# Kernel optimization log

Measured on AMD Instinct MI355X. Metric: run time of the kernel, lower is better.

The kernel has to match this reference:

```python
import jax, jax.numpy as jnp
import numpy as np

E = 8        # num experts
K = 2        # top-k
H = 1024     # hidden size
F = 3584     # intermediate (ffn) size
B, S = 1, 2048


def setup_inputs() -> dict:
    key = jax.random.key(0)
    ks = jax.random.split(key, 5)
    scale_h = 1.0 / np.sqrt(H)
    scale_f = 1.0 / np.sqrt(F)
    return {
        "hidden_states": jax.random.normal(ks[0], (B, S, H), jnp.float32),
        "gate_w": jax.random.normal(ks[1], (E, H), jnp.float32) * scale_h,  # Linear [out,in]
        "w1": jax.random.normal(ks[2], (E, F, H), jnp.float32) * scale_h,
        "w3": jax.random.normal(ks[3], (E, F, H), jnp.float32) * scale_h,
        "w2": jax.random.normal(ks[4], (E, H, F), jnp.float32) * scale_f,
    }


def reference(hidden_states, gate_w, w1, w3, w2):
    b, s, h = hidden_states.shape
    x = hidden_states.reshape(-1, h)                       # [T,H]
    T = x.shape[0]
    # Router: softmax over experts, top-k, renormalize
    router_logits = x @ gate_w.T                           # [T,E]
    routing_weights = jax.nn.softmax(router_logits.astype(jnp.float32), axis=-1)
    topk_w, topk_idx = jax.lax.top_k(routing_weights, K)   # [T,K]
    topk_w = topk_w / jnp.sum(topk_w, axis=-1, keepdims=True)
    # Per-token, per-expert combine weight (0 for unselected experts) --
    # matches the original mask-and-sum over all experts.
    tok = jnp.arange(T)
    expert_weights = jnp.zeros((T, E), jnp.float32).at[tok[:, None], topk_idx].add(topk_w)  # [T,E]
    # Dense per-expert SiLU-gated MLP over all tokens (as the reference loop does),
    # vectorized across experts.
    g = jnp.einsum("th,efh->etf", x, w1)                   # [E,T,F]
    u = jnp.einsum("th,efh->etf", x, w3)                   # [E,T,F]
    act = jax.nn.silu(g) * u                               # [E,T,F]
    y = jnp.einsum("etf,ehf->eth", act, w2)                # [E,T,H]
    out = jnp.einsum("eth,te->th", y, expert_weights.astype(y.dtype))  # [T,H]
    return out.reshape(b, s, h)
```

## Files before the change

### kernel.cpp

```cpp
#include <hip/hip_runtime.h>
#include <hip/hip_bf16.h>

#define T_TOK 2048
#define HID   1024
#define FF    3584
#define NE    8
#define TOPK  2
#define GRIDY 40

typedef __bf16 bf16x8 __attribute__((ext_vector_type(8)));
typedef float  f32x4  __attribute__((ext_vector_type(4)));
typedef unsigned short u16x8 __attribute__((ext_vector_type(8)));

#define WS_COUNTS   0u
#define WS_OFFSETS  64u
#define WS_TILECNT  128u
#define WS_TLE      256u
#define WS_TLM      512u
#define WS_TOPKI    1024u
#define WS_TOPKW    17408u
#define WS_SLOTPOS  33792u
#define WS_SLOTROW  50176u
#define WS_ROUTETOK 66560u
#define WS_XBF      131072u
#define WS_ACT      (WS_XBF + 2048u*1024u*2u)
#define WS_Y        (WS_ACT + 4096u*3584u*2u)

static __device__ __forceinline__ unsigned short f2bf(float f) {
    unsigned int u = __builtin_bit_cast(unsigned int, f);
    u += 0x7FFFu + ((u >> 16) & 1u);
    return (unsigned short)(u >> 16);
}
static __device__ __forceinline__ unsigned int pack2(float a, float b) {
    unsigned int ua = __builtin_bit_cast(unsigned int, a) + 0x8000u;
    unsigned int ub = __builtin_bit_cast(unsigned int, b) + 0x8000u;
    return (ua >> 16) | (ub & 0xFFFF0000u);
}

__global__ void k_cvt_x(const float* __restrict__ x, unsigned short* __restrict__ xb) {
    int i = blockIdx.x * blockDim.x + threadIdx.x;
    float4 v = ((const float4*)x)[i];
    ushort4 o;
    o.x = f2bf(v.x); o.y = f2bf(v.y); o.z = f2bf(v.z); o.w = f2bf(v.w);
    ((ushort4*)xb)[i] = o;
}

__global__ void k_router(const float* __restrict__ x, const float* __restrict__ gw,
                         int* __restrict__ counts, int* __restrict__ topki,
                         float* __restrict__ topkw, int* __restrict__ slotpos) {
    int t = blockIdx.x;
    int l = threadIdx.x;
    const float* xr = x + (size_t)t * HID;
    float acc[NE];
#pragma unroll
    for (int e = 0; e < NE; ++e) acc[e] = 0.f;
#pragma unroll
    for (int i = 0; i < HID / 64; ++i) {
        int h = l + 64 * i;
        float xv = xr[h];
#pragma unroll
        for (int e = 0; e < NE; ++e) acc[e] += xv * gw[e * HID + h];
    }
#pragma unroll
    for (int e = 0; e < NE; ++e) {
#pragma unroll
        for (int off = 32; off; off >>= 1) acc[e] += __shfl_xor(acc[e], off);
    }
    if (l == 0) {
        float best = -1e30f, second = -1e30f;
        int bi = 0, si = 0;
#pragma unroll
        for (int e = 0; e < NE; ++e) {
            float v = acc[e];
            if (v > best) { second = best; si = bi; best = v; bi = e; }
            else if (v > second) { second = v; si = e; }
        }
        float w0 = 1.f / (1.f + __expf(second - best));
        float w1 = 1.f - w0;
        topki[2 * t] = bi;  topki[2 * t + 1] = si;
        topkw[2 * t] = w0;  topkw[2 * t + 1] = w1;
        slotpos[2 * t]     = atomicAdd(&counts[bi], 1);
        slotpos[2 * t + 1] = atomicAdd(&counts[si], 1);
    }
}

__global__ void k_prefix(const int* __restrict__ counts, int* __restrict__ offsets,
                         int* __restrict__ tle, int* __restrict__ tlm,
                         int* __restrict__ tilecnt) {
    if (threadIdx.x == 0) {
        int o = 0;
#pragma unroll
        for (int e = 0; e < NE; ++e) { offsets[e] = o; o += counts[e]; }
        int n = 0;
        for (int e = 0; e < NE; ++e) {
            int t = (counts[e] + 127) >> 7;
            for (int i = 0; i < t; ++i) { tle[n] = e; tlm[n] = i; ++n; }
        }
        tilecnt[0] = n;
    }
}

__global__ void k_fill(const int* __restrict__ topki, const int* __restrict__ slotpos,
                       const int* __restrict__ offsets, int* __restrict__ routetok,
                       int* __restrict__ slotrow) {
    int j = blockIdx.x * blockDim.x + threadIdx.x;
    if (j >= T_TOK * TOPK) return;
    int e = topki[j];
    int row = offsets[e] + slotpos[j];
    routetok[row] = j >> 1;
    slotrow[j] = row;
}

__global__ __launch_bounds__(256) void k_gemm1(
    const unsigned short* __restrict__ xb, const float* __restrict__ w1,
    const float* __restrict__ w3, const int* __restrict__ counts,
    const int* __restrict__ offsets, const int* __restrict__ routetok,
    const int* __restrict__ tle, const int* __restrict__ tlm,
    const int* __restrict__ tilecnt, unsigned short* __restrict__ act)
{
    int by = blockIdx.y;
    if (by >= tilecnt[0]) return;
    int e = tle[by], mtile = tlm[by];
    int cnt = counts[e], obase = offsets[e];
    int rbase = mtile * 128;
    int fbase = blockIdx.x * 64;

    __shared__ __align__(16) unsigned short lA[128 * 72];
    __shared__ __align__(16) unsigned short lB1[64 * 72];
    __shared__ __align__(16) unsigned short lB3[64 * 72];
    __shared__ int ltok[128];

    int tid = threadIdx.x;
    if (tid < 128) {
        int r = rbase + tid;
        ltok[tid] = (r < cnt) ? routetok[obase + r] : 0;
    }
    __syncthreads();

    const int ra0 = tid >> 3, ca = (tid & 7) * 8;
    const int rb0 = tid >> 4, cb = (tid & 15) * 4;
    const unsigned short* pa[4];
    const float* pb1[4];
    const float* pb3[4];
    const float* w1e = w1 + ((size_t)e * FF + fbase) * HID;
    const float* w3e = w3 + ((size_t)e * FF + fbase) * HID;
#pragma unroll
    for (int i = 0; i < 4; ++i) {
        pa[i]  = xb + (size_t)ltok[ra0 + 32 * i] * HID + ca;
        pb1[i] = w1e + (size_t)(rb0 + 16 * i) * HID + cb;
        pb3[i] = w3e + (size_t)(rb0 + 16 * i) * HID + cb;
    }

    int lane = tid & 63, wv = tid >> 6, wr = wv >> 1, wc = wv & 1;
    f32x4 accg[4][2], accu[4][2];
#pragma unroll
    for (int m = 0; m < 4; ++m)
#pragma unroll
        for (int n = 0; n < 2; ++n) {
            accg[m][n] = (f32x4){0.f, 0.f, 0.f, 0.f};
            accu[m][n] = (f32x4){0.f, 0.f, 0.f, 0.f};
        }

    u16x8 ra[4]; float4 r1[4], r3[4];
#pragma unroll
    for (int i = 0; i < 4; ++i) {
        ra[i] = *(const u16x8*)(pa[i]);
        r1[i] = *(const float4*)(pb1[i]);
        r3[i] = *(const float4*)(pb3[i]);
    }

    for (int kt = 0; kt < HID / 64; ++kt) {
#pragma unroll
        for (int i = 0; i < 4; ++i) {
            *(u16x8*)(lA + (ra0 + 32 * i) * 72 + ca) = ra[i];
            uint2 p1; p1.x = pack2(r1[i].x, r1[i].y); p1.y = pack2(r1[i].z, r1[i].w);
            uint2 p3; p3.x = pack2(r3[i].x, r3[i].y); p3.y = pack2(r3[i].z, r3[i].w);
            *(uint2*)(lB1 + (rb0 + 16 * i) * 72 + cb) = p1;
            *(uint2*)(lB3 + (rb0 + 16 * i) * 72 + cb) = p3;
        }
        __syncthreads();
        if (kt < HID / 64 - 1) {
            int kof = (kt + 1) * 64;
#pragma unroll
            for (int i = 0; i < 4; ++i) {
                ra[i] = *(const u16x8*)(pa[i] + kof);
                r1[i] = *(const float4*)(pb1[i] + kof);
                r3[i] = *(const float4*)(pb3[i] + kof);
            }
        }
#pragma unroll
        for (int kk = 0; kk < 64; kk += 32) {
            int kcol = kk + (lane >> 4) * 8;
            bf16x8 a[4], b1[2], b3[2];
#pragma unroll
            for (int m = 0; m < 4; ++m)
                a[m] = *(const bf16x8*)(lA + (wr * 64 + m * 16 + (lane & 15)) * 72 + kcol);
#pragma unroll
            for (int n = 0; n < 2; ++n) {
                b1[n] = *(const bf16x8*)(lB1 + (wc * 32 + n * 16 + (lane & 15)) * 72 + kcol);
                b3[n] = *(const bf16x8*)(lB3 + (wc * 32 + n * 16 + (lane & 15)) * 72 + kcol);
            }
#pragma unroll
            for (int m = 0; m < 4; ++m)
#pragma unroll
                for (int n = 0; n < 2; ++n) {
                    accg[m][n] = __builtin_amdgcn_mfma_f32_16x16x32_bf16(a[m], b1[n], accg[m][n], 0, 0, 0);
                    accu[m][n] = __builtin_amdgcn_mfma_f32_16x16x32_bf16(a[m], b3[n], accu[m][n], 0, 0, 0);
                }
        }
        __syncthreads();
    }

#pragma unroll
    for (int m = 0; m < 4; ++m)
#pragma unroll
        for (int n = 0; n < 2; ++n)
#pragma unroll
            for (int r = 0; r < 4; ++r) {
                int lr = wr * 64 + m * 16 + (lane >> 4) * 4 + r;
                if (rbase + lr < cnt) {
                    float g = accg[m][n][r], u = accu[m][n][r];
                    float s = g / (1.f + __expf(-g));
                    int col = fbase + wc * 32 + n * 16 + (lane & 15);
                    act[(size_t)(obase + rbase + lr) * FF + col] = f2bf(s * u);
                }
            }
}

__global__ __launch_bounds__(256) void k_gemm2(
    const unsigned short* __restrict__ act, const float* __restrict__ w2,
    const int* __restrict__ counts, const int* __restrict__ offsets,
    const int* __restrict__ tle, const int* __restrict__ tlm,
    const int* __restrict__ tilecnt, float* __restrict__ y)
{
    int by = blockIdx.y;
    if (by >= tilecnt[0]) return;
    int e = tle[by], mtile = tlm[by];
    int cnt = counts[e], obase = offsets[e];
    int rbase = mtile * 128;
    int hbase = blockIdx.x * 64;
    int z = blockIdx.z;
    const int KS = FF / 64 / 2;

    __shared__ __align__(16) unsigned short lA[128 * 72];
    __shared__ __align__(16) unsigned short lB[64 * 72];

    int tid = threadIdx.x;
    const int ra0 = tid >> 3, ca = (tid & 7) * 8;
    const int rb0 = tid >> 4, cb = (tid & 15) * 4;
    const unsigned short* pa[4];
    const float* pb[4];
    const float* w2e = w2 + ((size_t)e * HID + hbase) * FF;
    int kbase0 = z * KS * 64;
#pragma unroll
    for (int i = 0; i < 4; ++i) {
        int rowg = obase + rbase + ra0 + 32 * i;
        if (rowg > 4095) rowg = 4095;
        pa[i] = act + (size_t)rowg * FF + ca + kbase0;
        pb[i] = w2e + (size_t)(rb0 + 16 * i) * FF + cb + kbase0;
    }

    int lane = tid & 63, wv = tid >> 6, wr = wv >> 1, wc = wv & 1;
    f32x4 acc[4][2];
#pragma unroll
    for (int m = 0; m < 4; ++m)
#pragma unroll
        for (int n = 0; n < 2; ++n) acc[m][n] = (f32x4){0.f, 0.f, 0.f, 0.f};

    u16x8 ra[4]; float4 rb[4];
#pragma unroll
    for (int i = 0; i < 4; ++i) {
        ra[i] = *(const u16x8*)(pa[i]);
        rb[i] = *(const float4*)(pb[i]);
    }

    for (int kt = 0; kt < KS; ++kt) {
#pragma unroll
        for (int i = 0; i < 4; ++i) {
            *(u16x8*)(lA + (ra0 + 32 * i) * 72 + ca) = ra[i];
            uint2 p; p.x = pack2(rb[i].x, rb[i].y); p.y = pack2(rb[i].z, rb[i].w);
            *(uint2*)(lB + (rb0 + 16 * i) * 72 + cb) = p;
        }
        __syncthreads();
        if (kt < KS - 1) {
            int kof = (kt + 1) * 64;
#pragma unroll
            for (int i = 0; i < 4; ++i) {
                ra[i] = *(const u16x8*)(pa[i] + kof);
                rb[i] = *(const float4*)(pb[i] + kof);
            }
        }
#pragma unroll
        for (int kk = 0; kk < 64; kk += 32) {
            int kcol = kk + (lane >> 4) * 8;
            bf16x8 a[4], b[2];
#pragma unroll
            for (int m = 0; m < 4; ++m)
                a[m] = *(const bf16x8*)(lA + (wr * 64 + m * 16 + (lane & 15)) * 72 + kcol);
#pragma unroll
            for (int n = 0; n < 2; ++n)
                b[n] = *(const bf16x8*)(lB + (wc * 32 + n * 16 + (lane & 15)) * 72 + kcol);
#pragma unroll
            for (int m = 0; m < 4; ++m)
#pragma unroll
                for (int n = 0; n < 2; ++n)
                    acc[m][n] = __builtin_amdgcn_mfma_f32_16x16x32_bf16(a[m], b[n], acc[m][n], 0, 0, 0);
        }
        __syncthreads();
    }

    float* yz = y + (size_t)z * T_TOK * TOPK * HID;
#pragma unroll
    for (int m = 0; m < 4; ++m)
#pragma unroll
        for (int n = 0; n < 2; ++n)
#pragma unroll
            for (int r = 0; r < 4; ++r) {
                int lr = wr * 64 + m * 16 + (lane >> 4) * 4 + r;
                if (rbase + lr < cnt) {
                    int col = hbase + wc * 32 + n * 16 + (lane & 15);
                    yz[(size_t)(obase + rbase + lr) * HID + col] = acc[m][n][r];
                }
            }
}

__global__ void k_combine(const float* __restrict__ y, const int* __restrict__ slotrow,
                          const float* __restrict__ topkw, float* __restrict__ out) {
    int j = blockIdx.x * blockDim.x + threadIdx.x;
    int t = j >> 8, c = j & 255;
    int r0 = slotrow[2 * t], r1 = slotrow[2 * t + 1];
    float w0 = topkw[2 * t], w1 = topkw[2 * t + 1];
    const float4* y0 = (const float4*)y;
    const float4* y1 = (const float4*)(y + (size_t)T_TOK * TOPK * HID);
    float4 a0 = y0[(size_t)r0 * 256 + c], a1 = y1[(size_t)r0 * 256 + c];
    float4 b0 = y0[(size_t)r1 * 256 + c], b1 = y1[(size_t)r1 * 256 + c];
    float4 o;
    o.x = w0 * (a0.x + a1.x) + w1 * (b0.x + b1.x);
    o.y = w0 * (a0.y + a1.y) + w1 * (b0.y + b1.y);
    o.z = w0 * (a0.z + a1.z) + w1 * (b0.z + b1.z);
    o.w = w0 * (a0.w + a1.w) + w1 * (b0.w + b1.w);
    ((float4*)out)[j] = o;
}

extern "C" void kernel_launch(void* const* d_in, const int* in_sizes, int n_in,
                              void* d_out, int out_size, void* d_ws, size_t ws_size,
                              hipStream_t stream) {
    const float* x  = (const float*)d_in[0];
    const float* gw = (const float*)d_in[1];
    const float* w1 = (const float*)d_in[2];
    const float* w3 = (const float*)d_in[3];
    const float* w2 = (const float*)d_in[4];
    float* out = (float*)d_out;

    char* ws = (char*)d_ws;
    int*   counts   = (int*)(ws + WS_COUNTS);
    int*   offsets  = (int*)(ws + WS_OFFSETS);
    int*   tilecnt  = (int*)(ws + WS_TILECNT);
    int*   tle      = (int*)(ws + WS_TLE);
    int*   tlm      = (int*)(ws + WS_TLM);
    int*   topki    = (int*)(ws + WS_TOPKI);
    float* topkw    = (float*)(ws + WS_TOPKW);
    int*   slotpos  = (int*)(ws + WS_SLOTPOS);
    int*   slotrow  = (int*)(ws + WS_SLOTROW);
    int*   routetok = (int*)(ws + WS_ROUTETOK);
    unsigned short* xb   = (unsigned short*)(ws + WS_XBF);
    unsigned short* actb = (unsigned short*)(ws + WS_ACT);
    float* yb = (float*)(ws + WS_Y);

    hipMemsetAsync(counts, 0, 64, stream);
    k_cvt_x<<<2048, 256, 0, stream>>>(x, xb);
    k_router<<<T_TOK, 64, 0, stream>>>(x, gw, counts, topki, topkw, slotpos);
    k_prefix<<<1, 64, 0, stream>>>(counts, offsets, tle, tlm, tilecnt);
    k_fill<<<16, 256, 0, stream>>>(topki, slotpos, offsets, routetok, slotrow);
    k_gemm1<<<dim3(FF / 64, GRIDY, 1), 256, 0, stream>>>(xb, w1, w3, counts, offsets, routetok, tle, tlm, tilecnt, actb);
    k_gemm2<<<dim3(HID / 64, GRIDY, 2), 256, 0, stream>>>(actb, w2, counts, offsets, tle, tlm, tilecnt, yb);
    k_combine<<<2048, 256, 0, stream>>>(yb, slotrow, topkw, out);
}
```

Measured before the change: 285.5 us.

## Enlarge MoE GEMM tiles, load activations directly to registers, fuse x cast into router

Both expert GEMMs are retiled with larger per-expert M tiles (512 rows for gate/up, 256 for down) and 512-thread blocks. The A operand (tokens or activations) is now loaded straight from global memory into MFMA registers instead of staged through LDS. Only the fp32 weights still go through LDS, so each weight tile is reused across more tokens. The x-to-bf16 conversion is folded into the router kernel, which now processes four tokens per block, removing one launch. The trade-offs are heavier register use (16 accumulator tiles each for gate and up), uncoalesced gathered A loads, and fewer blocks, which may hurt occupancy when tiles are partly empty.

```diff
diff --git a/kernel.cpp b/kernel.cpp
--- a/kernel.cpp
+++ b/kernel.cpp
@@ -6,7 +6,6 @@
 #define FF    3584
 #define NE    8
 #define TOPK  2
-#define GRIDY 40
 
 typedef __bf16 bf16x8 __attribute__((ext_vector_type(8)));
 typedef float  f32x4  __attribute__((ext_vector_type(4)));
@@ -15,13 +14,15 @@
 #define WS_COUNTS   0u
 #define WS_OFFSETS  64u
 #define WS_TILECNT  128u
-#define WS_TLE      256u
-#define WS_TLM      512u
-#define WS_TOPKI    1024u
-#define WS_TOPKW    17408u
-#define WS_SLOTPOS  33792u
-#define WS_SLOTROW  50176u
-#define WS_ROUTETOK 66560u
+#define WS_TLE1     256u
+#define WS_TLM1     512u
+#define WS_TLE2     768u
+#define WS_TLM2     1024u
+#define WS_TOPKI    4096u
+#define WS_TOPKW    20480u
+#define WS_SLOTPOS  36864u
+#define WS_SLOTROW  53248u
+#define WS_ROUTETOK 69632u
 #define WS_XBF      131072u
 #define WS_ACT      (WS_XBF + 2048u*1024u*2u)
 #define WS_Y        (WS_ACT + 4096u*3584u*2u)
@@ -37,29 +38,30 @@
     return (ua >> 16) | (ub & 0xFFFF0000u);
 }
 
-__global__ void k_cvt_x(const float* __restrict__ x, unsigned short* __restrict__ xb) {
-    int i = blockIdx.x * blockDim.x + threadIdx.x;
-    float4 v = ((const float4*)x)[i];
-    ushort4 o;
-    o.x = f2bf(v.x); o.y = f2bf(v.y); o.z = f2bf(v.z); o.w = f2bf(v.w);
-    ((ushort4*)xb)[i] = o;
-}
-
-__global__ void k_router(const float* __restrict__ x, const float* __restrict__ gw,
-                         int* __restrict__ counts, int* __restrict__ topki,
-                         float* __restrict__ topkw, int* __restrict__ slotpos) {
-    int t = blockIdx.x;
-    int l = threadIdx.x;
+__global__ __launch_bounds__(256) void k_router(
+    const float* __restrict__ x, const float* __restrict__ gw,
+    unsigned short* __restrict__ xb, int* __restrict__ counts,
+    int* __restrict__ topki, float* __restrict__ topkw, int* __restrict__ slotpos)
+{
+    int t = blockIdx.x * 4 + (threadIdx.x >> 6);
+    int l = threadIdx.x & 63;
     const float* xr = x + (size_t)t * HID;
+    unsigned short* xbr = xb + (size_t)t * HID;
     float acc[NE];
 #pragma unroll
     for (int e = 0; e < NE; ++e) acc[e] = 0.f;
 #pragma unroll
-    for (int i = 0; i < HID / 64; ++i) {
-        int h = l + 64 * i;
-        float xv = xr[h];
-#pragma unroll
-        for (int e = 0; e < NE; ++e) acc[e] += xv * gw[e * HID + h];
+    for (int i = 0; i < 4; ++i) {
+        int h = l * 4 + i * 256;
+        float4 xv = *(const float4*)(xr + h);
+        ushort4 o;
+        o.x = f2bf(xv.x); o.y = f2bf(xv.y); o.z = f2bf(xv.z); o.w = f2bf(xv.w);
+        *(ushort4*)(xbr + h) = o;
+#pragma unroll
+        for (int e = 0; e < NE; ++e) {
+            float4 g = *(const float4*)(gw + e * HID + h);
+            acc[e] += xv.x * g.x + xv.y * g.y + xv.z * g.z + xv.w * g.w;
+        }
     }
 #pragma unroll
     for (int e = 0; e < NE; ++e) {
@@ -85,18 +87,21 @@
 }
 
 __global__ void k_prefix(const int* __restrict__ counts, int* __restrict__ offsets,
-                         int* __restrict__ tle, int* __restrict__ tlm,
+                         int* __restrict__ tl1e, int* __restrict__ tl1m,
+                         int* __restrict__ tl2e, int* __restrict__ tl2m,
                          int* __restrict__ tilecnt) {
     if (threadIdx.x == 0) {
         int o = 0;
 #pragma unroll
         for (int e = 0; e < NE; ++e) { offsets[e] = o; o += counts[e]; }
-        int n = 0;
+        int n1 = 0, n2 = 0;
         for (int e = 0; e < NE; ++e) {
-            int t = (counts[e] + 127) >> 7;
-            for (int i = 0; i < t; ++i) { tle[n] = e; tlm[n] = i; ++n; }
-        }
-        tilecnt[0] = n;
+            int t1 = (counts[e] + 511) >> 9;
+            for (int i = 0; i < t1; ++i) { tl1e[n1] = e; tl1m[n1] = i; ++n1; }
+            int t2 = (counts[e] + 255) >> 8;
+            for (int i = 0; i < t2; ++i) { tl2e[n2] = e; tl2m[n2] = i; ++n2; }
+        }
+        tilecnt[0] = n1; tilecnt[1] = n2;
     }
 }
 
@@ -111,101 +116,117 @@
     slotrow[j] = row;
 }
 
-__global__ __launch_bounds__(256) void k_gemm1(
+__global__ __launch_bounds__(512, 2) void k_gemm1(
     const unsigned short* __restrict__ xb, const float* __restrict__ w1,
     const float* __restrict__ w3, const int* __restrict__ counts,
     const int* __restrict__ offsets, const int* __restrict__ routetok,
-    const int* __restrict__ tle, const int* __restrict__ tlm,
+    const int* __restrict__ tl1e, const int* __restrict__ tl1m,
     const int* __restrict__ tilecnt, unsigned short* __restrict__ act)
 {
     int by = blockIdx.y;
     if (by >= tilecnt[0]) return;
-    int e = tle[by], mtile = tlm[by];
+    int e = tl1e[by];
+    int rbase = tl1m[by] * 512;
     int cnt = counts[e], obase = offsets[e];
-    int rbase = mtile * 128;
     int fbase = blockIdx.x * 64;
 
-    __shared__ __align__(16) unsigned short lA[128 * 72];
     __shared__ __align__(16) unsigned short lB1[64 * 72];
     __shared__ __align__(16) unsigned short lB3[64 * 72];
-    __shared__ int ltok[128];
+    __shared__ int ltok[512];
 
     int tid = threadIdx.x;
-    if (tid < 128) {
+    {
         int r = rbase + tid;
-        ltok[tid] = (r < cnt) ? routetok[obase + r] : 0;
+        int rc = r < cnt ? r : cnt - 1;
+        ltok[tid] = routetok[obase + rc];
     }
     __syncthreads();
 
-    const int ra0 = tid >> 3, ca = (tid & 7) * 8;
-    const int rb0 = tid >> 4, cb = (tid & 15) * 4;
-    const unsigned short* pa[4];
-    const float* pb1[4];
-    const float* pb3[4];
-    const float* w1e = w1 + ((size_t)e * FF + fbase) * HID;
-    const float* w3e = w3 + ((size_t)e * FF + fbase) * HID;
-#pragma unroll
-    for (int i = 0; i < 4; ++i) {
-        pa[i]  = xb + (size_t)ltok[ra0 + 32 * i] * HID + ca;
-        pb1[i] = w1e + (size_t)(rb0 + 16 * i) * HID + cb;
-        pb3[i] = w3e + (size_t)(rb0 + 16 * i) * HID + cb;
-    }
-
-    int lane = tid & 63, wv = tid >> 6, wr = wv >> 1, wc = wv & 1;
-    f32x4 accg[4][2], accu[4][2];
+    int lane = tid & 63, wv = tid >> 6;
+    int klane = (lane >> 4) * 8;
+    const char* xbb = (const char*)xb;
+    unsigned int aoff[4];
 #pragma unroll
     for (int m = 0; m < 4; ++m)
-#pragma unroll
-        for (int n = 0; n < 2; ++n) {
+        aoff[m] = (unsigned int)ltok[wv * 64 + m * 16 + (lane & 15)] * (HID * 2);
+
+    int rbr = tid >> 3, cbc = (tid & 7) * 8;
+    const float* pb1 = w1 + ((size_t)e * FF + fbase + rbr) * HID + cbc;
+    const float* pb3 = w3 + ((size_t)e * FF + fbase + rbr) * HID + cbc;
+
+    f32x4 accg[4][4], accu[4][4];
+#pragma unroll
+    for (int m = 0; m < 4; ++m)
+#pragma unroll
+        for (int n = 0; n < 4; ++n) {
             accg[m][n] = (f32x4){0.f, 0.f, 0.f, 0.f};
             accu[m][n] = (f32x4){0.f, 0.f, 0.f, 0.f};
         }
 
-    u16x8 ra[4]; float4 r1[4], r3[4];
-#pragma unroll
-    for (int i = 0; i < 4; ++i) {
-        ra[i] = *(const u16x8*)(pa[i]);
-        r1[i] = *(const float4*)(pb1[i]);
-        r3[i] = *(const float4*)(pb3[i]);
-    }
+    float4 r1a = *(const float4*)(pb1);
+    float4 r1b = *(const float4*)(pb1 + 4);
+    float4 r3a = *(const float4*)(pb3);
+    float4 r3b = *(const float4*)(pb3 + 4);
+    u16x8 a0[4], a1[4];
+#pragma unroll
+    for (int m = 0; m < 4; ++m)
+        a0[m] = *(const u16x8*)(xbb + aoff[m] + klane * 2);
 
     for (int kt = 0; kt < HID / 64; ++kt) {
-#pragma unroll
-        for (int i = 0; i < 4; ++i) {
-            *(u16x8*)(lA + (ra0 + 32 * i) * 72 + ca) = ra[i];
-            uint2 p1; p1.x = pack2(r1[i].x, r1[i].y); p1.y = pack2(r1[i].z, r1[i].w);
-            uint2 p3; p3.x = pack2(r3[i].x, r3[i].y); p3.y = pack2(r3[i].z, r3[i].w);
-            *(uint2*)(lB1 + (rb0 + 16 * i) * 72 + cb) = p1;
-            *(uint2*)(lB3 + (rb0 + 16 * i) * 72 + cb) = p3;
-        }
+        uint2 p;
+        p.x = pack2(r1a.x, r1a.y); p.y = pack2(r1a.z, r1a.w);
+        *(uint2*)(lB1 + rbr * 72 + cbc) = p;
+        p.x = pack2(r1b.x, r1b.y); p.y = pack2(r1b.z, r1b.w);
+        *(uint2*)(lB1 + rbr * 72 + cbc + 4) = p;
+        p.x = pack2(r3a.x, r3a.y); p.y = pack2(r3a.z, r3a.w);
+        *(uint2*)(lB3 + rbr * 72 + cbc) = p;
+        p.x = pack2(r3b.x, r3b.y); p.y = pack2(r3b.z, r3b.w);
+        *(uint2*)(lB3 + rbr * 72 + cbc + 4) = p;
         __syncthreads();
+
+        int kof = (kt + 1) * 64;
         if (kt < HID / 64 - 1) {
-            int kof = (kt + 1) * 64;
-#pragma unroll
-            for (int i = 0; i < 4; ++i) {
-                ra[i] = *(const u16x8*)(pa[i] + kof);
-                r1[i] = *(const float4*)(pb1[i] + kof);
-                r3[i] = *(const float4*)(pb3[i] + kof);
+            r1a = *(const float4*)(pb1 + kof);
+            r1b = *(const float4*)(pb1 + kof + 4);
+            r3a = *(const float4*)(pb3 + kof);
+            r3b = *(const float4*)(pb3 + kof + 4);
+        }
+#pragma unroll
+        for (int m = 0; m < 4; ++m)
+            a1[m] = *(const u16x8*)(xbb + aoff[m] + (kt * 64 + 32 + klane) * 2);
+        {
+            bf16x8 b1f[4], b3f[4];
+#pragma unroll
+            for (int n = 0; n < 4; ++n) {
+                b1f[n] = *(const bf16x8*)(lB1 + (n * 16 + (lane & 15)) * 72 + klane);
+                b3f[n] = *(const bf16x8*)(lB3 + (n * 16 + (lane & 15)) * 72 + klane);
             }
-        }
-#pragma unroll
-        for (int kk = 0; kk < 64; kk += 32) {
-            int kcol = kk + (lane >> 4) * 8;
-            bf16x8 a[4], b1[2], b3[2];
 #pragma unroll
             for (int m = 0; m < 4; ++m)
-                a[m] = *(const bf16x8*)(lA + (wr * 64 + m * 16 + (lane & 15)) * 72 + kcol);
-#pragma unroll
-            for (int n = 0; n < 2; ++n) {
-                b1[n] = *(const bf16x8*)(lB1 + (wc * 32 + n * 16 + (lane & 15)) * 72 + kcol);
-                b3[n] = *(const bf16x8*)(lB3 + (wc * 32 + n * 16 + (lane & 15)) * 72 + kcol);
+#pragma unroll
+                for (int n = 0; n < 4; ++n) {
+                    accg[m][n] = __builtin_amdgcn_mfma_f32_16x16x32_bf16(a0[m], b1f[n], accg[m][n], 0, 0, 0);
+                    accu[m][n] = __builtin_amdgcn_mfma_f32_16x16x32_bf16(a0[m], b3f[n], accu[m][n], 0, 0, 0);
+                }
+        }
+        if (kt < HID / 64 - 1) {
+#pragma unroll
+            for (int m = 0; m < 4; ++m)
+                a0[m] = *(const u16x8*)(xbb + aoff[m] + (kof + klane) * 2);
+        }
+        {
+            bf16x8 b1f[4], b3f[4];
+#pragma unroll
+            for (int n = 0; n < 4; ++n) {
+                b1f[n] = *(const bf16x8*)(lB1 + (n * 16 + (lane & 15)) * 72 + 32 + klane);
+                b3f[n] = *(const bf16x8*)(lB3 + (n * 16 + (lane & 15)) * 72 + 32 + klane);
             }
 #pragma unroll
             for (int m = 0; m < 4; ++m)
 #pragma unroll
-                for (int n = 0; n < 2; ++n) {
-                    accg[m][n] = __builtin_amdgcn_mfma_f32_16x16x32_bf16(a[m], b1[n], accg[m][n], 0, 0, 0);
-                    accu[m][n] = __builtin_amdgcn_mfma_f32_16x16x32_bf16(a[m], b3[n], accu[m][n], 0, 0, 0);
+                for (int n = 0; n < 4; ++n) {
+                    accg[m][n] = __builtin_amdgcn_mfma_f32_16x16x32_bf16(a1[m], b1f[n], accg[m][n], 0, 0, 0);
+                    accu[m][n] = __builtin_amdgcn_mfma_f32_16x16x32_bf16(a1[m], b3f[n], accu[m][n], 0, 0, 0);
                 }
         }
         __syncthreads();
@@ -214,111 +235,129 @@
 #pragma unroll
     for (int m = 0; m < 4; ++m)
 #pragma unroll
-        for (int n = 0; n < 2; ++n)
+        for (int n = 0; n < 4; ++n)
 #pragma unroll
             for (int r = 0; r < 4; ++r) {
-                int lr = wr * 64 + m * 16 + (lane >> 4) * 4 + r;
+                int lr = wv * 64 + m * 16 + (lane >> 4) * 4 + r;
                 if (rbase + lr < cnt) {
                     float g = accg[m][n][r], u = accu[m][n][r];
                     float s = g / (1.f + __expf(-g));
-                    int col = fbase + wc * 32 + n * 16 + (lane & 15);
+                    int col = fbase + n * 16 + (lane & 15);
                     act[(size_t)(obase + rbase + lr) * FF + col] = f2bf(s * u);
                 }
             }
 }
 
-__global__ __launch_bounds__(256) void k_gemm2(
+__global__ __launch_bounds__(512, 2) void k_gemm2(
     const unsigned short* __restrict__ act, const float* __restrict__ w2,
     const int* __restrict__ counts, const int* __restrict__ offsets,
-    const int* __restrict__ tle, const int* __restrict__ tlm,
+    const int* __restrict__ tl2e, const int* __restrict__ tl2m,
     const int* __restrict__ tilecnt, float* __restrict__ y)
 {
     int by = blockIdx.y;
-    if (by >= tilecnt[0]) return;
-    int e = tle[by], mtile = tlm[by];
+    if (by >= tilecnt[1]) return;
+    int e = tl2e[by];
+    int rbase = tl2m[by] * 256;
     int cnt = counts[e], obase = offsets[e];
-    int rbase = mtile * 128;
-    int hbase = blockIdx.x * 64;
+    int hbase = blockIdx.x * 128;
     int z = blockIdx.z;
-    const int KS = FF / 64 / 2;
-
-    __shared__ __align__(16) unsigned short lA[128 * 72];
-    __shared__ __align__(16) unsigned short lB[64 * 72];
-
-    int tid = threadIdx.x;
-    const int ra0 = tid >> 3, ca = (tid & 7) * 8;
-    const int rb0 = tid >> 4, cb = (tid & 15) * 4;
-    const unsigned short* pa[4];
-    const float* pb[4];
-    const float* w2e = w2 + ((size_t)e * HID + hbase) * FF;
-    int kbase0 = z * KS * 64;
-#pragma unroll
-    for (int i = 0; i < 4; ++i) {
-        int rowg = obase + rbase + ra0 + 32 * i;
-        if (rowg > 4095) rowg = 4095;
-        pa[i] = act + (size_t)rowg * FF + ca + kbase0;
-        pb[i] = w2e + (size_t)(rb0 + 16 * i) * FF + cb + kbase0;
-    }
-
-    int lane = tid & 63, wv = tid >> 6, wr = wv >> 1, wc = wv & 1;
-    f32x4 acc[4][2];
-#pragma unroll
-    for (int m = 0; m < 4; ++m)
-#pragma unroll
-        for (int n = 0; n < 2; ++n) acc[m][n] = (f32x4){0.f, 0.f, 0.f, 0.f};
-
-    u16x8 ra[4]; float4 rb[4];
-#pragma unroll
-    for (int i = 0; i < 4; ++i) {
-        ra[i] = *(const u16x8*)(pa[i]);
-        rb[i] = *(const float4*)(pb[i]);
-    }
+    const int kb0 = z * (FF / 2);
+    const int KS = FF / 2 / 64;
+
+    __shared__ __align__(16) unsigned short lB[128 * 72];
+
+    int tid = threadIdx.x, lane = tid & 63, wv = tid >> 6;
+    int klane = (lane >> 4) * 8;
+
+    int rbr = tid >> 2, cbc = (tid & 3) * 16;
+    const float* pb = w2 + ((size_t)e * HID + hbase + rbr) * FF + kb0 + cbc;
+
+    const char* actb = (const char*)act;
+    unsigned int aoff[2];
+#pragma unroll
+    for (int m = 0; m < 2; ++m) {
+        int r = obase + rbase + wv * 32 + m * 16 + (lane & 15);
+        if (r > 4095) r = 4095;
+        aoff[m] = (unsigned int)r * (FF * 2);
+    }
+
+    f32x4 acc[2][8];
+#pragma unroll
+    for (int m = 0; m < 2; ++m)
+#pragma unroll
+        for (int n = 0; n < 8; ++n) acc[m][n] = (f32x4){0.f, 0.f, 0.f, 0.f};
+
+    float4 rw0 = *(const float4*)(pb);
+    float4 rw1 = *(const float4*)(pb + 4);
+    float4 rw2 = *(const float4*)(pb + 8);
+    float4 rw3 = *(const float4*)(pb + 12);
+    u16x8 a0[2], a1[2];
+#pragma unroll
+    for (int m = 0; m < 2; ++m)
+        a0[m] = *(const u16x8*)(actb + aoff[m] + (kb0 + klane) * 2);
 
     for (int kt = 0; kt < KS; ++kt) {
-#pragma unroll
-        for (int i = 0; i < 4; ++i) {
-            *(u16x8*)(lA + (ra0 + 32 * i) * 72 + ca) = ra[i];
-            uint2 p; p.x = pack2(rb[i].x, rb[i].y); p.y = pack2(rb[i].z, rb[i].w);
-            *(uint2*)(lB + (rb0 + 16 * i) * 72 + cb) = p;
-        }
+        uint2 p;
+        p.x = pack2(rw0.x, rw0.y); p.y = pack2(rw0.z, rw0.w);
+        *(uint2*)(lB + rbr * 72 + cbc) = p;
+        p.x = pack2(rw1.x, rw1.y); p.y = pack2(rw1.z, rw1.w);
+        *(uint2*)(lB + rbr * 72 + cbc + 4) = p;
+        p.x = pack2(rw2.x, rw2.y); p.y = pack2(rw2.z, rw2.w);
+        *(uint2*)(lB + rbr * 72 + cbc + 8) = p;
+        p.x = pack2(rw3.x, rw3.y); p.y = pack2(rw3.z, rw3.w);
+        *(uint2*)(lB + rbr * 72 + cbc + 12) = p;
         __syncthreads();
+
+        int kof = (kt + 1) * 64;
         if (kt < KS - 1) {
-            int kof = (kt + 1) * 64;
-#pragma unroll
-            for (int i = 0; i < 4; ++i) {
-                ra[i] = *(const u16x8*)(pa[i] + kof);
-                rb[i] = *(const float4*)(pb[i] + kof);
-            }
-        }
-#pragma unroll
-        for (int kk = 0; kk < 64; kk += 32) {
-            int kcol = kk + (lane >> 4) * 8;
-            bf16x8 a[4], b[2];
-#pragma unroll
-            for (int m = 0; m < 4; ++m)
-                a[m] = *(const bf16x8*)(lA + (wr * 64 + m * 16 + (lane & 15)) * 72 + kcol);
-#pragma unroll
-            for (int n = 0; n < 2; ++n)
-                b[n] = *(const bf16x8*)(lB + (wc * 32 + n * 16 + (lane & 15)) * 72 + kcol);
-#pragma unroll
-            for (int m = 0; m < 4; ++m)
-#pragma unroll
-                for (int n = 0; n < 2; ++n)
-                    acc[m][n] = __builtin_amdgcn_mfma_f32_16x16x32_bf16(a[m], b[n], acc[m][n], 0, 0, 0);
+            rw0 = *(const float4*)(pb + kof);
+            rw1 = *(const float4*)(pb + kof + 4);
+            rw2 = *(const float4*)(pb + kof + 8);
+            rw3 = *(const float4*)(pb + kof + 12);
+        }
+#pragma unroll
+        for (int m = 0; m < 2; ++m)
+            a1[m] = *(const u16x8*)(actb + aoff[m] + (kb0 + kt * 64 + 32 + klane) * 2);
+        {
+            bf16x8 bf[8];
+#pragma unroll
+            for (int n = 0; n < 8; ++n)
+                bf[n] = *(const bf16x8*)(lB + (n * 16 + (lane & 15)) * 72 + klane);
+#pragma unroll
+            for (int m = 0; m < 2; ++m)
+#pragma unroll
+                for (int n = 0; n < 8; ++n)
+                    acc[m][n] = __builtin_amdgcn_mfma_f32_16x16x32_bf16(a0[m], bf[n], acc[m][n], 0, 0, 0);
+        }
+        if (kt < KS - 1) {
+#pragma unroll
+            for (int m = 0; m < 2; ++m)
+                a0[m] = *(const u16x8*)(actb + aoff[m] + (kb0 + kof + klane) * 2);
+        }
+        {
+            bf16x8 bf[8];
+#pragma unroll
+            for (int n = 0; n < 8; ++n)
+                bf[n] = *(const bf16x8*)(lB + (n * 16 + (lane & 15)) * 72 + 32 + klane);
+#pragma unroll
+            for (int m = 0; m < 2; ++m)
+#pragma unroll
+                for (int n = 0; n < 8; ++n)
+                    acc[m][n] = __builtin_amdgcn_mfma_f32_16x16x32_bf16(a1[m], bf[n], acc[m][n], 0, 0, 0);
         }
         __syncthreads();
     }
 
-    float* yz = y + (size_t)z * T_TOK * TOPK * HID;
-#pragma unroll
-    for (int m = 0; m < 4; ++m)
-#pragma unroll
-        for (int n = 0; n < 2; ++n)
+    float* yz = y + (size_t)z * (T_TOK * TOPK * HID);
+#pragma unroll
+    for (int m = 0; m < 2; ++m)
+#pragma unroll
+        for (int n = 0; n < 8; ++n)
 #pragma unroll
             for (int r = 0; r < 4; ++r) {
-                int lr = wr * 64 + m * 16 + (lane >> 4) * 4 + r;
+                int lr = wv * 32 + m * 16 + (lane >> 4) * 4 + r;
                 if (rbase + lr < cnt) {
-                    int col = hbase + wc * 32 + n * 16 + (lane & 15);
+                    int col = hbase + n * 16 + (lane & 15);
                     yz[(size_t)(obase + rbase + lr) * HID + col] = acc[m][n][r];
                 }
             }
@@ -356,8 +395,10 @@
     int*   counts   = (int*)(ws + WS_COUNTS);
     int*   offsets  = (int*)(ws + WS_OFFSETS);
     int*   tilecnt  = (int*)(ws + WS_TILECNT);
-    int*   tle      = (int*)(ws + WS_TLE);
-    int*   tlm      = (int*)(ws + WS_TLM);
+    int*   tl1e     = (int*)(ws + WS_TLE1);
+    int*   tl1m     = (int*)(ws + WS_TLM1);
+    int*   tl2e     = (int*)(ws + WS_TLE2);
+    int*   tl2m     = (int*)(ws + WS_TLM2);
     int*   topki    = (int*)(ws + WS_TOPKI);
     float* topkw    = (float*)(ws + WS_TOPKW);
     int*   slotpos  = (int*)(ws + WS_SLOTPOS);
@@ -368,11 +409,10 @@
     float* yb = (float*)(ws + WS_Y);
 
     hipMemsetAsync(counts, 0, 64, stream);
-    k_cvt_x<<<2048, 256, 0, stream>>>(x, xb);
-    k_router<<<T_TOK, 64, 0, stream>>>(x, gw, counts, topki, topkw, slotpos);
-    k_prefix<<<1, 64, 0, stream>>>(counts, offsets, tle, tlm, tilecnt);
+    k_router<<<T_TOK / 4, 256, 0, stream>>>(x, gw, xb, counts, topki, topkw, slotpos);
+    k_prefix<<<1, 64, 0, stream>>>(counts, offsets, tl1e, tl1m, tl2e, tl2m, tilecnt);
     k_fill<<<16, 256, 0, stream>>>(topki, slotpos, offsets, routetok, slotrow);
-    k_gemm1<<<dim3(FF / 64, GRIDY, 1), 256, 0, stream>>>(xb, w1, w3, counts, offsets, routetok, tle, tlm, tilecnt, actb);
-    k_gemm2<<<dim3(HID / 64, GRIDY, 2), 256, 0, stream>>>(actb, w2, counts, offsets, tle, tlm, tilecnt, yb);
+    k_gemm1<<<dim3(FF / 64, 16, 1), 512, 0, stream>>>(xb, w1, w3, counts, offsets, routetok, tl1e, tl1m, tilecnt, actb);
+    k_gemm2<<<dim3(HID / 128, 24, 2), 512, 0, stream>>>(actb, w2, counts, offsets, tl2e, tl2m, tilecnt, yb);
     k_combine<<<2048, 256, 0, stream>>>(yb, slotrow, topkw, out);
 }
```

Result: slower. 355.5 us (+24.5%).

## Double MoE GEMM row tiles to 256, pre-gather routed tokens, vectorize router

Applied to the files above, without the earlier changes.

Both expert GEMMs now use 256-row M tiles with 512-thread blocks instead of 128-row tiles with 256 threads. The tile list and grid height shrink to match, so each expert's fp32 weights are re-read from memory by fewer tiles. A new gather kernel writes routed tokens as contiguous bf16 rows, replacing the full x conversion and the per-tile indirect token lookup. The router now handles four tokens per block using float4 loads. In exchange the blocks need more LDS and registers, and padding in partially filled 256-row tiles wastes more compute.

```diff
diff --git a/kernel.cpp b/kernel.cpp
--- a/kernel.cpp
+++ b/kernel.cpp
@@ -6,7 +6,7 @@
 #define FF    3584
 #define NE    8
 #define TOPK  2
-#define GRIDY 40
+#define GRIDY 24
 
 typedef __bf16 bf16x8 __attribute__((ext_vector_type(8)));
 typedef float  f32x4  __attribute__((ext_vector_type(4)));
@@ -17,13 +17,13 @@
 #define WS_TILECNT  128u
 #define WS_TLE      256u
 #define WS_TLM      512u
-#define WS_TOPKI    1024u
-#define WS_TOPKW    17408u
-#define WS_SLOTPOS  33792u
-#define WS_SLOTROW  50176u
-#define WS_ROUTETOK 66560u
-#define WS_XBF      131072u
-#define WS_ACT      (WS_XBF + 2048u*1024u*2u)
+#define WS_TOPKI    4096u
+#define WS_TOPKW    20480u
+#define WS_SLOTPOS  36864u
+#define WS_SLOTROW  53248u
+#define WS_ROUTETOK 69632u
+#define WS_XG       131072u
+#define WS_ACT      (WS_XG + 4096u*1024u*2u)
 #define WS_Y        (WS_ACT + 4096u*3584u*2u)
 
 static __device__ __forceinline__ unsigned short f2bf(float f) {
@@ -37,29 +37,26 @@
     return (ua >> 16) | (ub & 0xFFFF0000u);
 }
 
-__global__ void k_cvt_x(const float* __restrict__ x, unsigned short* __restrict__ xb) {
-    int i = blockIdx.x * blockDim.x + threadIdx.x;
-    float4 v = ((const float4*)x)[i];
-    ushort4 o;
-    o.x = f2bf(v.x); o.y = f2bf(v.y); o.z = f2bf(v.z); o.w = f2bf(v.w);
-    ((ushort4*)xb)[i] = o;
-}
-
-__global__ void k_router(const float* __restrict__ x, const float* __restrict__ gw,
-                         int* __restrict__ counts, int* __restrict__ topki,
-                         float* __restrict__ topkw, int* __restrict__ slotpos) {
-    int t = blockIdx.x;
-    int l = threadIdx.x;
+__global__ __launch_bounds__(256) void k_router(
+    const float* __restrict__ x, const float* __restrict__ gw,
+    int* __restrict__ counts, int* __restrict__ topki,
+    float* __restrict__ topkw, int* __restrict__ slotpos)
+{
+    int t = blockIdx.x * 4 + (threadIdx.x >> 6);
+    int l = threadIdx.x & 63;
     const float* xr = x + (size_t)t * HID;
     float acc[NE];
 #pragma unroll
     for (int e = 0; e < NE; ++e) acc[e] = 0.f;
 #pragma unroll
-    for (int i = 0; i < HID / 64; ++i) {
-        int h = l + 64 * i;
-        float xv = xr[h];
-#pragma unroll
-        for (int e = 0; e < NE; ++e) acc[e] += xv * gw[e * HID + h];
+    for (int i = 0; i < 4; ++i) {
+        int h = l * 4 + i * 256;
+        float4 xv = *(const float4*)(xr + h);
+#pragma unroll
+        for (int e = 0; e < NE; ++e) {
+            float4 g = *(const float4*)(gw + e * HID + h);
+            acc[e] += xv.x * g.x + xv.y * g.y + xv.z * g.z + xv.w * g.w;
+        }
     }
 #pragma unroll
     for (int e = 0; e < NE; ++e) {
@@ -93,7 +90,7 @@
         for (int e = 0; e < NE; ++e) { offsets[e] = o; o += counts[e]; }
         int n = 0;
         for (int e = 0; e < NE; ++e) {
-            int t = (counts[e] + 127) >> 7;
+            int t = (counts[e] + 255) >> 8;
             for (int i = 0; i < t; ++i) { tle[n] = e; tlm[n] = i; ++n; }
         }
         tilecnt[0] = n;
@@ -111,47 +108,58 @@
     slotrow[j] = row;
 }
 
-__global__ __launch_bounds__(256) void k_gemm1(
-    const unsigned short* __restrict__ xb, const float* __restrict__ w1,
+__global__ void k_gather(const float* __restrict__ x, const int* __restrict__ routetok,
+                         unsigned short* __restrict__ xg) {
+    int j = blockIdx.x * blockDim.x + threadIdx.x;
+    int r = j >> 8;
+    int c = (j & 255) * 4;
+    int tok = routetok[r];
+    float4 v = *(const float4*)(x + (size_t)tok * HID + c);
+    ushort4 o;
+    o.x = f2bf(v.x); o.y = f2bf(v.y); o.z = f2bf(v.z); o.w = f2bf(v.w);
+    *(ushort4*)(xg + (size_t)r * HID + c) = o;
+}
+
+__global__ __launch_bounds__(512, 4) void k_gemm1(
+    const unsigned short* __restrict__ xg, const float* __restrict__ w1,
     const float* __restrict__ w3, const int* __restrict__ counts,
-    const int* __restrict__ offsets, const int* __restrict__ routetok,
-    const int* __restrict__ tle, const int* __restrict__ tlm,
-    const int* __restrict__ tilecnt, unsigned short* __restrict__ act)
+    const int* __restrict__ offsets, const int* __restrict__ tle,
+    const int* __restrict__ tlm, const int* __restrict__ tilecnt,
+    unsigned short* __restrict__ act)
 {
     int by = blockIdx.y;
     if (by >= tilecnt[0]) return;
-    int e = tle[by], mtile = tlm[by];
+    int e = tle[by];
+    int rbase = tlm[by] * 256;
     int cnt = counts[e], obase = offsets[e];
-    int rbase = mtile * 128;
     int fbase = blockIdx.x * 64;
 
-    __shared__ __align__(16) unsigned short lA[128 * 72];
+    __shared__ __align__(16) unsigned short lA[256 * 72];
     __shared__ __align__(16) unsigned short lB1[64 * 72];
     __shared__ __align__(16) unsigned short lB3[64 * 72];
-    __shared__ int ltok[128];
 
     int tid = threadIdx.x;
-    if (tid < 128) {
-        int r = rbase + tid;
-        ltok[tid] = (r < cnt) ? routetok[obase + r] : 0;
-    }
-    __syncthreads();
-
     const int ra0 = tid >> 3, ca = (tid & 7) * 8;
     const int rb0 = tid >> 4, cb = (tid & 15) * 4;
     const unsigned short* pa[4];
-    const float* pb1[4];
-    const float* pb3[4];
+#pragma unroll
+    for (int i = 0; i < 4; ++i) {
+        int r = obase + rbase + ra0 + 64 * i;
+        if (r > 4095) r = 4095;
+        pa[i] = xg + (size_t)r * HID + ca;
+    }
     const float* w1e = w1 + ((size_t)e * FF + fbase) * HID;
     const float* w3e = w3 + ((size_t)e * FF + fbase) * HID;
-#pragma unroll
-    for (int i = 0; i < 4; ++i) {
-        pa[i]  = xb + (size_t)ltok[ra0 + 32 * i] * HID + ca;
-        pb1[i] = w1e + (size_t)(rb0 + 16 * i) * HID + cb;
-        pb3[i] = w3e + (size_t)(rb0 + 16 * i) * HID + cb;
+    const float* pb1[2];
+    const float* pb3[2];
+#pragma unroll
+    for (int i = 0; i < 2; ++i) {
+        pb1[i] = w1e + (size_t)(rb0 + 32 * i) * HID + cb;
+        pb3[i] = w3e + (size_t)(rb0 + 32 * i) * HID + cb;
     }
 
     int lane = tid & 63, wv = tid >> 6, wr = wv >> 1, wc = wv & 1;
+    int klane = (lane >> 4) * 8;
     f32x4 accg[4][2], accu[4][2];
 #pragma unroll
     for (int m = 0; m < 4; ++m)
@@ -161,36 +169,38 @@
             accu[m][n] = (f32x4){0.f, 0.f, 0.f, 0.f};
         }
 
-    u16x8 ra[4]; float4 r1[4], r3[4];
-#pragma unroll
-    for (int i = 0; i < 4; ++i) {
-        ra[i] = *(const u16x8*)(pa[i]);
-        r1[i] = *(const float4*)(pb1[i]);
-        r3[i] = *(const float4*)(pb3[i]);
-    }
+    u16x8 ra[4]; float4 r1[2], r3[2];
+#pragma unroll
+    for (int i = 0; i < 4; ++i) ra[i] = *(const u16x8*)(pa[i]);
+#pragma unroll
+    for (int i = 0; i < 2; ++i) { r1[i] = *(const float4*)(pb1[i]); r3[i] = *(const float4*)(pb3[i]); }
 
     for (int kt = 0; kt < HID / 64; ++kt) {
 #pragma unroll
-        for (int i = 0; i < 4; ++i) {
-            *(u16x8*)(lA + (ra0 + 32 * i) * 72 + ca) = ra[i];
-            uint2 p1; p1.x = pack2(r1[i].x, r1[i].y); p1.y = pack2(r1[i].z, r1[i].w);
-            uint2 p3; p3.x = pack2(r3[i].x, r3[i].y); p3.y = pack2(r3[i].z, r3[i].w);
-            *(uint2*)(lB1 + (rb0 + 16 * i) * 72 + cb) = p1;
-            *(uint2*)(lB3 + (rb0 + 16 * i) * 72 + cb) = p3;
+        for (int i = 0; i < 4; ++i)
+            *(u16x8*)(lA + (ra0 + 64 * i) * 72 + ca) = ra[i];
+#pragma unroll
+        for (int i = 0; i < 2; ++i) {
+            uint2 p;
+            p.x = pack2(r1[i].x, r1[i].y); p.y = pack2(r1[i].z, r1[i].w);
+            *(uint2*)(lB1 + (rb0 + 32 * i) * 72 + cb) = p;
+            p.x = pack2(r3[i].x, r3[i].y); p.y = pack2(r3[i].z, r3[i].w);
+            *(uint2*)(lB3 + (rb0 + 32 * i) * 72 + cb) = p;
         }
         __syncthreads();
         if (kt < HID / 64 - 1) {
             int kof = (kt + 1) * 64;
 #pragma unroll
-            for (int i = 0; i < 4; ++i) {
-                ra[i] = *(const u16x8*)(pa[i] + kof);
+            for (int i = 0; i < 4; ++i) ra[i] = *(const u16x8*)(pa[i] + kof);
+#pragma unroll
+            for (int i = 0; i < 2; ++i) {
                 r1[i] = *(const float4*)(pb1[i] + kof);
                 r3[i] = *(const float4*)(pb3[i] + kof);
             }
         }
 #pragma unroll
         for (int kk = 0; kk < 64; kk += 32) {
-            int kcol = kk + (lane >> 4) * 8;
+            int kcol = kk + klane;
             bf16x8 a[4], b1[2], b3[2];
 #pragma unroll
             for (int m = 0; m < 4; ++m)
@@ -227,7 +237,7 @@
             }
 }
 
-__global__ __launch_bounds__(256) void k_gemm2(
+__global__ __launch_bounds__(512, 4) void k_gemm2(
     const unsigned short* __restrict__ act, const float* __restrict__ w2,
     const int* __restrict__ counts, const int* __restrict__ offsets,
     const int* __restrict__ tle, const int* __restrict__ tlm,
@@ -235,64 +245,68 @@
 {
     int by = blockIdx.y;
     if (by >= tilecnt[0]) return;
-    int e = tle[by], mtile = tlm[by];
+    int e = tle[by];
+    int rbase = tlm[by] * 256;
     int cnt = counts[e], obase = offsets[e];
-    int rbase = mtile * 128;
     int hbase = blockIdx.x * 64;
     int z = blockIdx.z;
-    const int KS = FF / 64 / 2;
-
-    __shared__ __align__(16) unsigned short lA[128 * 72];
+    const int kb0 = z * (FF / 2);
+    const int KS = FF / 2 / 64;
+
+    __shared__ __align__(16) unsigned short lA[256 * 72];
     __shared__ __align__(16) unsigned short lB[64 * 72];
 
     int tid = threadIdx.x;
     const int ra0 = tid >> 3, ca = (tid & 7) * 8;
     const int rb0 = tid >> 4, cb = (tid & 15) * 4;
     const unsigned short* pa[4];
-    const float* pb[4];
+#pragma unroll
+    for (int i = 0; i < 4; ++i) {
+        int r = obase + rbase + ra0 + 64 * i;
+        if (r > 4095) r = 4095;
+        pa[i] = act + (size_t)r * FF + kb0 + ca;
+    }
     const float* w2e = w2 + ((size_t)e * HID + hbase) * FF;
-    int kbase0 = z * KS * 64;
-#pragma unroll
-    for (int i = 0; i < 4; ++i) {
-        int rowg = obase + rbase + ra0 + 32 * i;
-        if (rowg > 4095) rowg = 4095;
-        pa[i] = act + (size_t)rowg * FF + ca + kbase0;
-        pb[i] = w2e + (size_t)(rb0 + 16 * i) * FF + cb + kbase0;
-    }
+    const float* pb[2];
+#pragma unroll
+    for (int i = 0; i < 2; ++i)
+        pb[i] = w2e + (size_t)(rb0 + 32 * i) * FF + kb0 + cb;
 
     int lane = tid & 63, wv = tid >> 6, wr = wv >> 1, wc = wv & 1;
+    int klane = (lane >> 4) * 8;
     f32x4 acc[4][2];
 #pragma unroll
     for (int m = 0; m < 4; ++m)
 #pragma unroll
         for (int n = 0; n < 2; ++n) acc[m][n] = (f32x4){0.f, 0.f, 0.f, 0.f};
 
-    u16x8 ra[4]; float4 rb[4];
-#pragma unroll
-    for (int i = 0; i < 4; ++i) {
-        ra[i] = *(const u16x8*)(pa[i]);
-        rb[i] = *(const float4*)(pb[i]);
-    }
+    u16x8 ra[4]; float4 rw[2];
+#pragma unroll
+    for (int i = 0; i < 4; ++i) ra[i] = *(const u16x8*)(pa[i]);
+#pragma unroll
+    for (int i = 0; i < 2; ++i) rw[i] = *(const float4*)(pb[i]);
 
     for (int kt = 0; kt < KS; ++kt) {
 #pragma unroll
-        for (int i = 0; i < 4; ++i) {
-            *(u16x8*)(lA + (ra0 + 32 * i) * 72 + ca) = ra[i];
-            uint2 p; p.x = pack2(rb[i].x, rb[i].y); p.y = pack2(rb[i].z, rb[i].w);
-            *(uint2*)(lB + (rb0 + 16 * i) * 72 + cb) = p;
+        for (int i = 0; i < 4; ++i)
+            *(u16x8*)(lA + (ra0 + 64 * i) * 72 + ca) = ra[i];
+#pragma unroll
+        for (int i = 0; i < 2; ++i) {
+            uint2 p;
+            p.x = pack2(rw[i].x, rw[i].y); p.y = pack2(rw[i].z, rw[i].w);
+            *(uint2*)(lB + (rb0 + 32 * i) * 72 + cb) = p;
         }
         __syncthreads();
         if (kt < KS - 1) {
             int kof = (kt + 1) * 64;
 #pragma unroll
-            for (int i = 0; i < 4; ++i) {
-                ra[i] = *(const u16x8*)(pa[i] + kof);
-                rb[i] = *(const float4*)(pb[i] + kof);
-            }
+            for (int i = 0; i < 4; ++i) ra[i] = *(const u16x8*)(pa[i] + kof);
+#pragma unroll
+            for (int i = 0; i < 2; ++i) rw[i] = *(const float4*)(pb[i] + kof);
         }
 #pragma unroll
         for (int kk = 0; kk < 64; kk += 32) {
-            int kcol = kk + (lane >> 4) * 8;
+            int kcol = kk + klane;
             bf16x8 a[4], b[2];
 #pragma unroll
             for (int m = 0; m < 4; ++m)
@@ -309,7 +323,7 @@
         __syncthreads();
     }
 
-    float* yz = y + (size_t)z * T_TOK * TOPK * HID;
+    float* yz = y + (size_t)z * (T_TOK * TOPK * HID);
 #pragma unroll
     for (int m = 0; m < 4; ++m)
 #pragma unroll
@@ -363,16 +377,16 @@
     int*   slotpos  = (int*)(ws + WS_SLOTPOS);
     int*   slotrow  = (int*)(ws + WS_SLOTROW);
     int*   routetok = (int*)(ws + WS_ROUTETOK);
-    unsigned short* xb   = (unsigned short*)(ws + WS_XBF);
+    unsigned short* xg   = (unsigned short*)(ws + WS_XG);
     unsigned short* actb = (unsigned short*)(ws + WS_ACT);
     float* yb = (float*)(ws + WS_Y);
 
     hipMemsetAsync(counts, 0, 64, stream);
-    k_cvt_x<<<2048, 256, 0, stream>>>(x, xb);
-    k_router<<<T_TOK, 64, 0, stream>>>(x, gw, counts, topki, topkw, slotpos);
+    k_router<<<T_TOK / 4, 256, 0, stream>>>(x, gw, counts, topki, topkw, slotpos);
     k_prefix<<<1, 64, 0, stream>>>(counts, offsets, tle, tlm, tilecnt);
     k_fill<<<16, 256, 0, stream>>>(topki, slotpos, offsets, routetok, slotrow);
-    k_gemm1<<<dim3(FF / 64, GRIDY, 1), 256, 0, stream>>>(xb, w1, w3, counts, offsets, routetok, tle, tlm, tilecnt, actb);
-    k_gemm2<<<dim3(HID / 64, GRIDY, 2), 256, 0, stream>>>(actb, w2, counts, offsets, tle, tlm, tilecnt, yb);
+    k_gather<<<4096, 256, 0, stream>>>(x, routetok, xg);
+    k_gemm1<<<dim3(FF / 64, GRIDY, 1), 512, 0, stream>>>(xg, w1, w3, counts, offsets, tle, tlm, tilecnt, actb);
+    k_gemm2<<<dim3(HID / 64, GRIDY, 2), 512, 0, stream>>>(actb, w2, counts, offsets, tle, tlm, tilecnt, yb);
     k_combine<<<2048, 256, 0, stream>>>(yb, slotrow, topkw, out);
 }
```

New measurement: 292.3 us. +2.4%, slower.
